# Kernel optimization log

Measured on AMD Instinct MI355X. Metric: run time of the kernel, lower is better.

Reference implementation:

```python
import jax, jax.numpy as jnp
import numpy as np

N_NODES = 50000
N_EDGES = 800000
N_GRAPHS = 64
D = 90


def _kaiming_uniform(key, shape, fan_in):
    # kaiming_uniform_ with nonlinearity='relu': gain=sqrt(2), bound=gain*sqrt(3/fan_in)
    bound = np.sqrt(2.0) * np.sqrt(3.0 / fan_in)
    return jax.random.uniform(key, shape, jnp.float32, -bound, bound)


def setup_inputs() -> dict:
    key = jax.random.key(0)
    ks = jax.random.split(key, 16)
    x = jax.random.normal(ks[0], (N_NODES, D), jnp.float32)
    edge_index = jax.random.randint(ks[1], (2, N_EDGES), 0, N_NODES, jnp.int64)
    batch = jnp.sort(jax.random.randint(ks[2], (N_NODES,), 0, N_GRAPHS, jnp.int64))
    inp = {"x": x, "edge_index": edge_index, "batch": batch}
    # SAGEConv params: lin_l (neighbor path, with bias), lin_r (root path, no bias)
    for i, (kl, kr) in enumerate([(ks[3], ks[4]), (ks[5], ks[6]), (ks[7], ks[8])], start=1):
        inp[f"W{i}l"] = _kaiming_uniform(kl, (D, D), D)
        inp[f"b{i}"] = jnp.zeros((D,), jnp.float32)
        inp[f"W{i}r"] = _kaiming_uniform(kr, (D, D), D)
    inp["Wf1"] = _kaiming_uniform(ks[9], (32, D), D)
    inp["bf1"] = jnp.zeros((32,), jnp.float32)
    inp["Wf2"] = _kaiming_uniform(ks[10], (1, 32), 32)
    inp["bf2"] = jnp.zeros((1,), jnp.float32)
    return inp


def _sage_conv(x, src, dst, Wl, bl, Wr):
    # mean-aggregate neighbor messages x[src] at dst, then lin_l(agg) + lin_r(x)
    msg = x[src]                                           # [E, D] gather
    agg = jax.ops.segment_sum(msg, dst, num_segments=N_NODES)  # [N, D] scatter-add
    deg = jax.ops.segment_sum(jnp.ones((src.shape[0],), x.dtype), dst,
                              num_segments=N_NODES)
    agg = agg / jnp.maximum(deg, 1.0)[:, None]
    return agg @ Wl.T + bl + x @ Wr.T


def reference(x, edge_index, batch, W1l, b1, W1r, W2l, b2, W2r, W3l, b3, W3r,
              Wf1, bf1, Wf2, bf2):
    src, dst = edge_index[0], edge_index[1]
    h = jax.nn.relu(_sage_conv(x, src, dst, W1l, b1, W1r))
    h = jax.nn.relu(_sage_conv(h, src, dst, W2l, b2, W2r))
    h = jax.nn.relu(_sage_conv(h, src, dst, W3l, b3, W3r))
    # global_mean_pool over graph ids
    sums = jax.ops.segment_sum(h, batch, num_segments=N_GRAPHS)      # [G, D]
    cnts = jax.ops.segment_sum(jnp.ones((h.shape[0],), h.dtype), batch,
                               num_segments=N_GRAPHS)
    pooled = sums / jnp.maximum(cnts, 1.0)[:, None]
    h4 = jax.nn.relu(pooled @ Wf1.T + bf1)
    return h4 @ Wf2.T + bf2  # [G, 1]
```

## Files before the change

### kernel.cpp

```cpp
#include <hip/hip_runtime.h>
#include <hip/hip_bf16.h>

#define N_NODES 50000
#define N_PAD   50048
#define N_EDGES 800000
#define N_GRAPHS 64
#define D 90
#define HS  96
#define HSD 48
#define SC  192

#define NBUCKETS 196
#define BSHIFT 8
#define BIN_EPB 4096

typedef __attribute__((ext_vector_type(8))) short bf16x8;
typedef __attribute__((ext_vector_type(4))) float f32x4;

__device__ __forceinline__ float bflo(unsigned int v) { return __uint_as_float(v << 16); }
__device__ __forceinline__ float bfhi(unsigned int v) { return __uint_as_float(v & 0xffff0000u); }
__device__ __forceinline__ unsigned short bf16bits(float f) {
    __hip_bfloat16 b = __float2bfloat16(f);
    return *(unsigned short*)&b;
}
__device__ __forceinline__ unsigned int pack2bf(float lo, float hi) {
    return (unsigned int)bf16bits(lo) | ((unsigned int)bf16bits(hi) << 16);
}

__global__ void k_prep(const float* __restrict__ x, __hip_bfloat16* __restrict__ h0,
                       const float* __restrict__ w1l, const float* __restrict__ w1r,
                       const float* __restrict__ w2l, const float* __restrict__ w2r,
                       const float* __restrict__ w3l, const float* __restrict__ w3r,
                       __hip_bfloat16* __restrict__ Wcat,
                       int* __restrict__ bcnt, float* __restrict__ pooled) {
    int idx = blockIdx.x * 256 + threadIdx.x;
    if (idx < N_PAD * HS) {
        int n = idx / HS, k = idx - n * HS;
        float v = (n < N_NODES && k < D) ? x[n * D + k] : 0.f;
        h0[idx] = __float2bfloat16(v);
    }
    if (idx < 3 * 96 * SC) {
        const int per = 96 * SC;
        int layer = idx / per, rem = idx - layer * per;
        int j = rem / SC, k = rem - j * SC;
        const float* wl = (layer == 0) ? w1l : (layer == 1) ? w2l : w3l;
        const float* wr = (layer == 0) ? w1r : (layer == 1) ? w2r : w3r;
        float v = 0.f;
        if (j < D) {
            if (k < 96) { if (k < D) v = wl[j * D + k]; }
            else        { int kk = k - 96; if (kk < D) v = wr[j * D + kk]; }
        }
        Wcat[idx] = __float2bfloat16(v);
    }
    if (idx < N_GRAPHS * D + N_GRAPHS) pooled[idx] = 0.f;
    if (idx < NBUCKETS) bcnt[idx] = 0;
}

__global__ void k_hist(const int* __restrict__ dst, int* __restrict__ bcnt) {
    __shared__ int h[NBUCKETS];
    int t = threadIdx.x;
    for (int i = t; i < NBUCKETS; i += 256) h[i] = 0;
    __syncthreads();
    int base = blockIdx.x * BIN_EPB;
    int lim = base + BIN_EPB; if (lim > N_EDGES) lim = N_EDGES;
    for (int e = base + t; e < lim; e += 256)
        atomicAdd(&h[dst[e] >> BSHIFT], 1);
    __syncthreads();
    for (int i = t; i < NBUCKETS; i += 256) {
        int c = h[i];
        if (c) atomicAdd(&bcnt[i], c);
    }
}

__global__ void k_bscan(const int* __restrict__ bcnt, int* __restrict__ bbase,
                        int* __restrict__ bcursor) {
    __shared__ int s[256];
    int t = threadIdx.x;
    int v = (t < NBUCKETS) ? bcnt[t] : 0;
    s[t] = v; __syncthreads();
    for (int o = 1; o < 256; o <<= 1) {
        int x = (t >= o) ? s[t - o] : 0;
        __syncthreads();
        s[t] += x;
        __syncthreads();
    }
    int excl = s[t] - v;
    if (t < NBUCKETS) { bbase[t] = excl; bcursor[t] = excl; }
    if (t == 255) bbase[NBUCKETS] = s[255];
}

__global__ __launch_bounds__(256) void k_bin(const int* __restrict__ src,
                                             const int* __restrict__ dst,
                                             int* __restrict__ bcursor,
                                             unsigned int* __restrict__ ebuf) {
    __shared__ int h[NBUCKETS];
    __shared__ int gb[NBUCKETS];
    int t = threadIdx.x;
    for (int i = t; i < NBUCKETS; i += 256) h[i] = 0;
    __syncthreads();
    int base = blockIdx.x * BIN_EPB;
    int sv[16], dv[16], rv[16];
    #pragma unroll
    for (int i = 0; i < 16; ++i) {
        int e = base + i * 256 + t;
        if (e < N_EDGES) {
            sv[i] = src[e];
            dv[i] = dst[e];
            rv[i] = atomicAdd(&h[dv[i] >> BSHIFT], 1);
        }
    }
    __syncthreads();
    for (int i = t; i < NBUCKETS; i += 256)
        gb[i] = h[i] ? atomicAdd(&bcursor[i], h[i]) : 0;
    __syncthreads();
    #pragma unroll
    for (int i = 0; i < 16; ++i) {
        int e = base + i * 256 + t;
        if (e < N_EDGES) {
            int b = dv[i] >> BSHIFT;
            ebuf[gb[b] + rv[i]] = (unsigned int)sv[i] | ((unsigned int)(dv[i] & 255) << 16);
        }
    }
}

__global__ __launch_bounds__(256) void k_fill2(const unsigned int* __restrict__ ebuf,
                                               const int* __restrict__ bbase,
                                               int* __restrict__ off,
                                               int* __restrict__ csr) {
    __shared__ int lcnt[256];
    __shared__ int excl[256];
    int t = threadIdx.x;
    int n0 = blockIdx.x << BSHIFT;
    int ebeg = bbase[blockIdx.x], eend = bbase[blockIdx.x + 1];
    lcnt[t] = 0;
    __syncthreads();
    for (int e = ebeg + t; e < eend; e += 256)
        atomicAdd(&lcnt[ebuf[e] >> 16], 1);
    __syncthreads();
    int v = lcnt[t];
    excl[t] = v; __syncthreads();
    for (int o = 1; o < 256; o <<= 1) {
        int x = (t >= o) ? excl[t - o] : 0;
        __syncthreads();
        excl[t] += x;
        __syncthreads();
    }
    excl[t] -= v;
    int n = n0 + t;
    if (n <= N_NODES) off[n] = ebeg + excl[t];
    lcnt[t] = 0;
    __syncthreads();
    for (int e = ebeg + t; e < eend; e += 256) {
        unsigned int u = ebuf[e];
        int li = u >> 16;
        int r = atomicAdd(&lcnt[li], 1);
        csr[ebeg + excl[li] + r] = (int)(u & 0xFFFFu);
    }
}

__global__ __launch_bounds__(512) void k_layer(
    const unsigned int* __restrict__ hin,
    const __hip_bfloat16* __restrict__ Wcat,
    const float* __restrict__ bias,
    const int* __restrict__ off, const int* __restrict__ csr,
    __hip_bfloat16* __restrict__ hout)
{
    __shared__ unsigned int aggT[64][52];
    __shared__ float biasPad[96];
    int tid = threadIdx.x;
    if (tid < 96) biasPad[tid] = (tid < D) ? bias[tid] : 0.f;
    int w = tid >> 6, lane = tid & 63;

    int eg = lane >> 3, sl = lane & 7;
    int colw = 6 * sl;
    for (int i = 0; i < 8; ++i) {
        int local = w * 8 + i;
        int node = blockIdx.x * 64 + local;
        int beg = 0, end = 0;
        if (node < N_NODES) { beg = off[node]; end = off[node + 1]; }
        float a[12];
        #pragma unroll
        for (int q = 0; q < 12; ++q) a[q] = 0.f;
        int e = beg + eg;
        for (; e + 8 < end; e += 16) {
            int sA = csr[e], sB = csr[e + 8];
            const unsigned int* pA = &hin[sA * HSD + colw];
            const unsigned int* pB = &hin[sB * HSD + colw];
            unsigned int u[6], v[6];
            #pragma unroll
            for (int q = 0; q < 6; ++q) u[q] = pA[q];
            #pragma unroll
            for (int q = 0; q < 6; ++q) v[q] = pB[q];
            #pragma unroll
            for (int q = 0; q < 6; ++q) {
                a[2 * q]     += bflo(u[q]) + bflo(v[q]);
                a[2 * q + 1] += bfhi(u[q]) + bfhi(v[q]);
            }
        }
        if (e < end) {
            const unsigned int* pA = &hin[csr[e] * HSD + colw];
            unsigned int u[6];
            #pragma unroll
            for (int q = 0; q < 6; ++q) u[q] = pA[q];
            #pragma unroll
            for (int q = 0; q < 6; ++q) {
                a[2 * q]     += bflo(u[q]);
                a[2 * q + 1] += bfhi(u[q]);
            }
        }
        #pragma unroll
        for (int m = 8; m <= 32; m <<= 1) {
            #pragma unroll
            for (int q = 0; q < 12; ++q) a[q] += __shfl_xor(a[q], m);
        }
        if (eg == 0) {
            float inv = 1.0f / fmaxf((float)(end - beg), 1.0f);
            #pragma unroll
            for (int q = 0; q < 6; ++q) {
                int c0 = 12 * sl + 2 * q;
                float lo = (c0     < D) ? a[2 * q]     * inv : 0.f;
                float hi = (c0 + 1 < D) ? a[2 * q + 1] * inv : 0.f;
                aggT[local][colw + q] = pack2bf(lo, hi);
            }
        }
    }
    __syncthreads();

    int w4 = w & 3, half = w >> 2;
    int mrow = lane & 15, kg = lane >> 4;
    int r0 = blockIdx.x * 64 + w4 * 16;
    int lrow = w4 * 16 + mrow;
    const short* Wp = (const short*)Wcat;
    const short* Hs = (const short*)hin;

    f32x4 acc[3];
    #pragma unroll
    for (int t = 0; t < 3; ++t) {
        int j = (half * 3 + t) * 16 + mrow;
        float b = biasPad[j];
        acc[t] = (f32x4){b, b, b, b};
    }

    #pragma unroll
    for (int ks = 0; ks < 6; ++ks) {
        bf16x8 afr;
        if (ks < 3) afr = *(const bf16x8*)&aggT[lrow][ks * 16 + kg * 4];
        else        afr = *(const bf16x8*)&Hs[(r0 + mrow) * HS + (ks - 3) * 32 + kg * 8];
        #pragma unroll
        for (int t = 0; t < 3; ++t) {
            int j = (half * 3 + t) * 16 + mrow;
            bf16x8 bfr = *(const bf16x8*)&Wp[j * SC + ks * 32 + kg * 8];
            acc[t] = __builtin_amdgcn_mfma_f32_16x16x32_bf16(afr, bfr, acc[t], 0, 0, 0);
        }
    }

    int orow = r0 + kg * 4;
    #pragma unroll
    for (int t = 0; t < 3; ++t) {
        int j = (half * 3 + t) * 16 + mrow;
        #pragma unroll
        for (int v = 0; v < 4; ++v) {
            float val = (j < D) ? fmaxf(acc[t][v], 0.f) : 0.f;
            hout[(orow + v) * HS + j] = __float2bfloat16(val);
        }
    }
}

#define POOL_WAVES 4096
__global__ void k_pool(const unsigned int* __restrict__ h, const int* __restrict__ batch,
                       float* __restrict__ pooled, float* __restrict__ cntg) {
    int wid  = (blockIdx.x * blockDim.x + threadIdx.x) >> 6;
    int lane = threadIdx.x & 63;
    const int per = (N_NODES + POOL_WAVES - 1) / POOL_WAVES;
    int beg = wid * per;
    int end = beg + per; if (end > N_NODES) end = N_NODES;
    if (beg >= end) return;
    int cur = batch[beg];
    float a0 = 0.f, a1 = 0.f, c = 0.f;
    for (int n = beg; n < end; ++n) {
        int g = batch[n];
        if (g != cur) {
            if (lane < 45) {
                atomicAdd(&pooled[cur * D + 2 * lane], a0);
                atomicAdd(&pooled[cur * D + 2 * lane + 1], a1);
            }
            if (lane == 0) atomicAdd(&cntg[cur], c);
            a0 = a1 = c = 0.f;
            cur = g;
        }
        if (lane < 45) {
            unsigned int v = h[n * HSD + lane];
            a0 += bflo(v);
            a1 += bfhi(v);
        }
        c += 1.f;
    }
    if (lane < 45) {
        atomicAdd(&pooled[cur * D + 2 * lane], a0);
        atomicAdd(&pooled[cur * D + 2 * lane + 1], a1);
    }
    if (lane == 0) atomicAdd(&cntg[cur], c);
}

__global__ void k_mlp(const float* __restrict__ pooled, const float* __restrict__ cntg,
                      const float* __restrict__ Wf1, const float* __restrict__ bf1,
                      const float* __restrict__ Wf2, const float* __restrict__ bf2,
                      float* __restrict__ outp) {
    __shared__ float P[N_GRAPHS][92];
    __shared__ float H4[N_GRAPHS][32];
    int tid = threadIdx.x;
    for (int idx = tid; idx < N_GRAPHS * D; idx += 256) {
        int g = idx / D, d = idx - g * D;
        P[g][d] = pooled[idx] / fmaxf(cntg[g], 1.0f);
    }
    __syncthreads();
    for (int idx = tid; idx < N_GRAPHS * 32; idx += 256) {
        int g = idx >> 5, c = idx & 31;
        float acc = bf1[c];
        for (int d = 0; d < D; ++d) acc += P[g][d] * Wf1[c * D + d];
        H4[g][c] = fmaxf(acc, 0.f);
    }
    __syncthreads();
    if (tid < N_GRAPHS) {
        float acc = bf2[0];
        #pragma unroll
        for (int c = 0; c < 32; ++c) acc += H4[tid][c] * Wf2[c];
        outp[tid] = acc;
    }
}

extern "C" void kernel_launch(void* const* d_in, const int* in_sizes, int n_in,
                              void* d_out, int out_size, void* d_ws, size_t ws_size,
                              hipStream_t stream) {
    const float* x    = (const float*)d_in[0];
    const int*   ei   = (const int*)d_in[1];
    const int*   batch= (const int*)d_in[2];
    const float* W1l  = (const float*)d_in[3];
    const float* b1   = (const float*)d_in[4];
    const float* W1r  = (const float*)d_in[5];
    const float* W2l  = (const float*)d_in[6];
    const float* b2   = (const float*)d_in[7];
    const float* W2r  = (const float*)d_in[8];
    const float* W3l  = (const float*)d_in[9];
    const float* b3   = (const float*)d_in[10];
    const float* W3r  = (const float*)d_in[11];
    const float* Wf1  = (const float*)d_in[12];
    const float* bf1  = (const float*)d_in[13];
    const float* Wf2  = (const float*)d_in[14];
    const float* bf2  = (const float*)d_in[15];
    const int* srcI = ei;
    const int* dstI = ei + N_EDGES;

    char* base = (char*)d_ws;
    size_t o = 0;
    auto alloc = [&](size_t bytes) -> void* {
        void* p = base + o;
        o = (o + bytes + 255) & ~(size_t)255;
        return p;
    };
    int*   bcnt    = (int*)alloc((size_t)NBUCKETS * 4);
    int*   bbase   = (int*)alloc((size_t)(NBUCKETS + 1) * 4);
    int*   bcursor = (int*)alloc((size_t)NBUCKETS * 4);
    int*   off     = (int*)alloc((size_t)(N_NODES + 1) * 4);
    unsigned int* ebuf = (unsigned int*)alloc((size_t)N_EDGES * 4);
    int*   csr     = (int*)alloc((size_t)N_EDGES * 4);
    __hip_bfloat16* hA = (__hip_bfloat16*)alloc((size_t)N_PAD * HS * 2);
    __hip_bfloat16* hB = (__hip_bfloat16*)alloc((size_t)N_PAD * HS * 2);
    __hip_bfloat16* Wcat = (__hip_bfloat16*)alloc((size_t)3 * 96 * SC * 2);
    float* pooled = (float*)alloc((size_t)(N_GRAPHS * D + N_GRAPHS) * 4);
    float* cntg   = pooled + N_GRAPHS * D;

    k_prep<<<(N_PAD * HS + 255) / 256, 256, 0, stream>>>(
        x, hA, W1l, W1r, W2l, W2r, W3l, W3r, Wcat, bcnt, pooled);

    const int EB = (N_EDGES + BIN_EPB - 1) / BIN_EPB;
    k_hist<<<EB, 256, 0, stream>>>(dstI, bcnt);
    k_bscan<<<1, 256, 0, stream>>>(bcnt, bbase, bcursor);
    k_bin<<<EB, 256, 0, stream>>>(srcI, dstI, bcursor, ebuf);
    k_fill2<<<NBUCKETS, 256, 0, stream>>>(ebuf, bbase, off, csr);

    const int LAYER_BLOCKS = N_PAD / 64;

    unsigned int* hAu = (unsigned int*)hA;
    unsigned int* hBu = (unsigned int*)hB;

    k_layer<<<LAYER_BLOCKS, 512, 0, stream>>>(hAu, Wcat,            b1, off, csr, hB);
    k_layer<<<LAYER_BLOCKS, 512, 0, stream>>>(hBu, Wcat +  96 * SC, b2, off, csr, hA);
    k_layer<<<LAYER_BLOCKS, 512, 0, stream>>>(hAu, Wcat + 192 * SC, b3, off, csr, hB);

    k_pool<<<POOL_WAVES / 4, 256, 0, stream>>>(hBu, batch, pooled, cntg);
    k_mlp<<<1, 256, 0, stream>>>(pooled, cntg, Wf1, bf1, Wf2, bf2, (float*)d_out);
}
```

Measured before the change: 240.3 us.

## Store an fp8 copy of node features for the neighbor gather

Each layer now writes an fp8 shadow copy of its output features next to the bf16 copy, and the neighbor-aggregation gather reads the fp8 copy. This halves the bytes moved by the random-access gather, which is the dominant memory cost of the layer kernel. The root-path GEMM still reads bf16. The extra fp8 store adds write traffic and byte-granular stores, and fp8 loses a lot of precision, which may hurt accuracy.

```diff
diff --git a/kernel.cpp b/kernel.cpp
--- a/kernel.cpp
+++ b/kernel.cpp
@@ -8,6 +8,7 @@
 #define D 90
 #define HS  96
 #define HSD 48
+#define HS8 24
 #define SC  192
 
 #define NBUCKETS 196
@@ -16,6 +17,7 @@
 
 typedef __attribute__((ext_vector_type(8))) short bf16x8;
 typedef __attribute__((ext_vector_type(4))) float f32x4;
+typedef __attribute__((ext_vector_type(2))) float f32x2;
 
 __device__ __forceinline__ float bflo(unsigned int v) { return __uint_as_float(v << 16); }
 __device__ __forceinline__ float bfhi(unsigned int v) { return __uint_as_float(v & 0xffff0000u); }
@@ -26,8 +28,13 @@
 __device__ __forceinline__ unsigned int pack2bf(float lo, float hi) {
     return (unsigned int)bf16bits(lo) | ((unsigned int)bf16bits(hi) << 16);
 }
+__device__ __forceinline__ unsigned char f32_to_fp8(float v) {
+    int pk = __builtin_amdgcn_cvt_pk_fp8_f32(v, v, 0, false);
+    return (unsigned char)(pk & 0xff);
+}
 
 __global__ void k_prep(const float* __restrict__ x, __hip_bfloat16* __restrict__ h0,
+                       unsigned char* __restrict__ h8,
                        const float* __restrict__ w1l, const float* __restrict__ w1r,
                        const float* __restrict__ w2l, const float* __restrict__ w2r,
                        const float* __restrict__ w3l, const float* __restrict__ w3r,
@@ -38,6 +45,7 @@
         int n = idx / HS, k = idx - n * HS;
         float v = (n < N_NODES && k < D) ? x[n * D + k] : 0.f;
         h0[idx] = __float2bfloat16(v);
+        h8[idx] = f32_to_fp8(v);
     }
     if (idx < 3 * 96 * SC) {
         const int per = 96 * SC;
@@ -160,10 +168,12 @@
 
 __global__ __launch_bounds__(512) void k_layer(
     const unsigned int* __restrict__ hin,
+    const unsigned int* __restrict__ hin8,
     const __hip_bfloat16* __restrict__ Wcat,
     const float* __restrict__ bias,
     const int* __restrict__ off, const int* __restrict__ csr,
-    __hip_bfloat16* __restrict__ hout)
+    __hip_bfloat16* __restrict__ hout,
+    unsigned char* __restrict__ hout8)
 {
     __shared__ unsigned int aggT[64][52];
     __shared__ float biasPad[96];
@@ -172,7 +182,7 @@
     int w = tid >> 6, lane = tid & 63;
 
     int eg = lane >> 3, sl = lane & 7;
-    int colw = 6 * sl;
+    int col8 = 3 * sl;
     for (int i = 0; i < 8; ++i) {
         int local = w * 8 + i;
         int node = blockIdx.x * 64 + local;
@@ -181,33 +191,46 @@
         float a[12];
         #pragma unroll
         for (int q = 0; q < 12; ++q) a[q] = 0.f;
+
         int e = beg + eg;
         for (; e + 8 < end; e += 16) {
             int sA = csr[e], sB = csr[e + 8];
-            const unsigned int* pA = &hin[sA * HSD + colw];
-            const unsigned int* pB = &hin[sB * HSD + colw];
-            unsigned int u[6], v[6];
-            #pragma unroll
-            for (int q = 0; q < 6; ++q) u[q] = pA[q];
-            #pragma unroll
-            for (int q = 0; q < 6; ++q) v[q] = pB[q];
-            #pragma unroll
-            for (int q = 0; q < 6; ++q) {
-                a[2 * q]     += bflo(u[q]) + bflo(v[q]);
-                a[2 * q + 1] += bfhi(u[q]) + bfhi(v[q]);
+            const unsigned int* pA = &hin8[sA * HS8 + col8];
+            const unsigned int* pB = &hin8[sB * HS8 + col8];
+            unsigned int u[3], v[3];
+            #pragma unroll
+            for (int q = 0; q < 3; ++q) u[q] = pA[q];
+            #pragma unroll
+            for (int q = 0; q < 3; ++q) v[q] = pB[q];
+            #pragma unroll
+            for (int q = 0; q < 3; ++q) {
+                f32x2 lo = __builtin_amdgcn_cvt_pk_f32_fp8((int)u[q], false);
+                f32x2 hi = __builtin_amdgcn_cvt_pk_f32_fp8((int)u[q], true);
+                a[4 * q]     += lo.x; a[4 * q + 1] += lo.y;
+                a[4 * q + 2] += hi.x; a[4 * q + 3] += hi.y;
             }
+            #pragma unroll
+            for (int q = 0; q < 3; ++q) {
+                f32x2 lo = __builtin_amdgcn_cvt_pk_f32_fp8((int)v[q], false);
+                f32x2 hi = __builtin_amdgcn_cvt_pk_f32_fp8((int)v[q], true);
+                a[4 * q]     += lo.x; a[4 * q + 1] += lo.y;
+                a[4 * q + 2] += hi.x; a[4 * q + 3] += hi.y;
+            }
         }
         if (e < end) {
-            const unsigned int* pA = &hin[csr[e] * HSD + colw];
-            unsigned int u[6];
-            #pragma unroll
-            for (int q = 0; q < 6; ++q) u[q] = pA[q];
-            #pragma unroll
-            for (int q = 0; q < 6; ++q) {
-                a[2 * q]     += bflo(u[q]);
-                a[2 * q + 1] += bfhi(u[q]);
+            const unsigned int* pA = &hin8[csr[e] * HS8 + col8];
+            unsigned int u[3];
+            #pragma unroll
+            for (int q = 0; q < 3; ++q) u[q] = pA[q];
+            #pragma unroll
+            for (int q = 0; q < 3; ++q) {
+                f32x2 lo = __builtin_amdgcn_cvt_pk_f32_fp8((int)u[q], false);
+                f32x2 hi = __builtin_amdgcn_cvt_pk_f32_fp8((int)u[q], true);
+                a[4 * q]     += lo.x; a[4 * q + 1] += lo.y;
+                a[4 * q + 2] += hi.x; a[4 * q + 3] += hi.y;
             }
         }
+
         #pragma unroll
         for (int m = 8; m <= 32; m <<= 1) {
             #pragma unroll
@@ -220,7 +243,7 @@
                 int c0 = 12 * sl + 2 * q;
                 float lo = (c0     < D) ? a[2 * q]     * inv : 0.f;
                 float hi = (c0 + 1 < D) ? a[2 * q + 1] * inv : 0.f;
-                aggT[local][colw + q] = pack2bf(lo, hi);
+                aggT[local][6 * sl + q] = pack2bf(lo, hi);
             }
         }
     }
@@ -262,6 +285,7 @@
         for (int v = 0; v < 4; ++v) {
             float val = (j < D) ? fmaxf(acc[t][v], 0.f) : 0.f;
             hout[(orow + v) * HS + j] = __float2bfloat16(val);
+            hout8[(orow + v) * HS + j] = f32_to_fp8(val);
         }
     }
 }
@@ -366,12 +390,14 @@
     int*   csr     = (int*)alloc((size_t)N_EDGES * 4);
     __hip_bfloat16* hA = (__hip_bfloat16*)alloc((size_t)N_PAD * HS * 2);
     __hip_bfloat16* hB = (__hip_bfloat16*)alloc((size_t)N_PAD * HS * 2);
+    unsigned char* h8A = (unsigned char*)alloc((size_t)N_PAD * HS);
+    unsigned char* h8B = (unsigned char*)alloc((size_t)N_PAD * HS);
     __hip_bfloat16* Wcat = (__hip_bfloat16*)alloc((size_t)3 * 96 * SC * 2);
     float* pooled = (float*)alloc((size_t)(N_GRAPHS * D + N_GRAPHS) * 4);
     float* cntg   = pooled + N_GRAPHS * D;
 
     k_prep<<<(N_PAD * HS + 255) / 256, 256, 0, stream>>>(
-        x, hA, W1l, W1r, W2l, W2r, W3l, W3r, Wcat, bcnt, pooled);
+        x, hA, h8A, W1l, W1r, W2l, W2r, W3l, W3r, Wcat, bcnt, pooled);
 
     const int EB = (N_EDGES + BIN_EPB - 1) / BIN_EPB;
     k_hist<<<EB, 256, 0, stream>>>(dstI, bcnt);
@@ -381,12 +407,14 @@
 
     const int LAYER_BLOCKS = N_PAD / 64;
 
-    unsigned int* hAu = (unsigned int*)hA;
-    unsigned int* hBu = (unsigned int*)hB;
-
-    k_layer<<<LAYER_BLOCKS, 512, 0, stream>>>(hAu, Wcat,            b1, off, csr, hB);
-    k_layer<<<LAYER_BLOCKS, 512, 0, stream>>>(hBu, Wcat +  96 * SC, b2, off, csr, hA);
-    k_layer<<<LAYER_BLOCKS, 512, 0, stream>>>(hAu, Wcat + 192 * SC, b3, off, csr, hB);
+    unsigned int* hAu  = (unsigned int*)hA;
+    unsigned int* hBu  = (unsigned int*)hB;
+    unsigned int* h8Au = (unsigned int*)h8A;
+    unsigned int* h8Bu = (unsigned int*)h8B;
+
+    k_layer<<<LAYER_BLOCKS, 512, 0, stream>>>(hAu, h8Au, Wcat,            b1, off, csr, hB, h8B);
+    k_layer<<<LAYER_BLOCKS, 512, 0, stream>>>(hBu, h8Bu, Wcat +  96 * SC, b2, off, csr, hA, h8A);
+    k_layer<<<LAYER_BLOCKS, 512, 0, stream>>>(hAu, h8Au, Wcat + 192 * SC, b3, off, csr, hB, h8B);
 
     k_pool<<<POOL_WAVES / 4, 256, 0, stream>>>(hBu, batch, pooled, cntg);
     k_mlp<<<1, 256, 0, stream>>>(pooled, cntg, Wf1, bf1, Wf2, bf2, (float*)d_out);
```

Measured after the change: 248.3 us. +3.3%, slower.

## Assign one node per 8-lane group in layer aggregation, shrink blocks

Applied to the files above, without the earlier changes.

Layer aggregation now gives each node its own 8-lane group, which walks all of that node's edges serially with a 4-way unrolled gather. Previously the whole wave processed one node at a time, spreading edges across 8 groups and then reducing with cross-lane shuffles. The shuffle reduction and the serial per-node loop are removed, and blocks shrink to 32 nodes and 256 threads so the MFMA stage maps 2 row-tiles per block. The trade-off is that uneven degrees now cause load imbalance between groups in a wave, and each group holds more loads in flight.

```diff
diff --git a/kernel.cpp b/kernel.cpp
--- a/kernel.cpp
+++ b/kernel.cpp
@@ -158,78 +158,81 @@
     }
 }
 
-__global__ __launch_bounds__(512) void k_layer(
+__global__ __launch_bounds__(256) void k_layer(
     const unsigned int* __restrict__ hin,
     const __hip_bfloat16* __restrict__ Wcat,
     const float* __restrict__ bias,
     const int* __restrict__ off, const int* __restrict__ csr,
     __hip_bfloat16* __restrict__ hout)
 {
-    __shared__ unsigned int aggT[64][52];
+    __shared__ unsigned int aggT[32][52];
     __shared__ float biasPad[96];
     int tid = threadIdx.x;
     if (tid < 96) biasPad[tid] = (tid < D) ? bias[tid] : 0.f;
     int w = tid >> 6, lane = tid & 63;
 
-    int eg = lane >> 3, sl = lane & 7;
+    int grp = lane >> 3, sl = lane & 7;
+    int local = w * 8 + grp;
+    int node = blockIdx.x * 32 + local;
     int colw = 6 * sl;
-    for (int i = 0; i < 8; ++i) {
-        int local = w * 8 + i;
-        int node = blockIdx.x * 64 + local;
-        int beg = 0, end = 0;
-        if (node < N_NODES) { beg = off[node]; end = off[node + 1]; }
-        float a[12];
-        #pragma unroll
-        for (int q = 0; q < 12; ++q) a[q] = 0.f;
-        int e = beg + eg;
-        for (; e + 8 < end; e += 16) {
-            int sA = csr[e], sB = csr[e + 8];
-            const unsigned int* pA = &hin[sA * HSD + colw];
-            const unsigned int* pB = &hin[sB * HSD + colw];
-            unsigned int u[6], v[6];
-            #pragma unroll
-            for (int q = 0; q < 6; ++q) u[q] = pA[q];
-            #pragma unroll
-            for (int q = 0; q < 6; ++q) v[q] = pB[q];
-            #pragma unroll
-            for (int q = 0; q < 6; ++q) {
-                a[2 * q]     += bflo(u[q]) + bflo(v[q]);
-                a[2 * q + 1] += bfhi(u[q]) + bfhi(v[q]);
-            }
-        }
-        if (e < end) {
-            const unsigned int* pA = &hin[csr[e] * HSD + colw];
-            unsigned int u[6];
-            #pragma unroll
-            for (int q = 0; q < 6; ++q) u[q] = pA[q];
-            #pragma unroll
-            for (int q = 0; q < 6; ++q) {
-                a[2 * q]     += bflo(u[q]);
-                a[2 * q + 1] += bfhi(u[q]);
-            }
-        }
-        #pragma unroll
-        for (int m = 8; m <= 32; m <<= 1) {
-            #pragma unroll
-            for (int q = 0; q < 12; ++q) a[q] += __shfl_xor(a[q], m);
-        }
-        if (eg == 0) {
-            float inv = 1.0f / fmaxf((float)(end - beg), 1.0f);
-            #pragma unroll
-            for (int q = 0; q < 6; ++q) {
-                int c0 = 12 * sl + 2 * q;
-                float lo = (c0     < D) ? a[2 * q]     * inv : 0.f;
-                float hi = (c0 + 1 < D) ? a[2 * q + 1] * inv : 0.f;
-                aggT[local][colw + q] = pack2bf(lo, hi);
-            }
-        }
-    }
-    __syncthreads();
-
-    int w4 = w & 3, half = w >> 2;
+
+    int beg = 0, end = 0;
+    if (node < N_NODES) { beg = off[node]; end = off[node + 1]; }
+
+    float a[12];
+    #pragma unroll
+    for (int q = 0; q < 12; ++q) a[q] = 0.f;
+
+    int e = beg;
+    for (; e + 4 <= end; e += 4) {
+        int s0 = csr[e], s1 = csr[e + 1], s2 = csr[e + 2], s3 = csr[e + 3];
+        const unsigned int* p0 = &hin[s0 * HSD + colw];
+        const unsigned int* p1 = &hin[s1 * HSD + colw];
+        const unsigned int* p2 = &hin[s2 * HSD + colw];
+        const unsigned int* p3 = &hin[s3 * HSD + colw];
+        unsigned int u0[6], u1[6], u2[6], u3[6];
+        #pragma unroll
+        for (int q = 0; q < 6; ++q) u0[q] = p0[q];
+        #pragma unroll
+        for (int q = 0; q < 6; ++q) u1[q] = p1[q];
+        #pragma unroll
+        for (int q = 0; q < 6; ++q) u2[q] = p2[q];
+        #pragma unroll
+        for (int q = 0; q < 6; ++q) u3[q] = p3[q];
+        #pragma unroll
+        for (int q = 0; q < 6; ++q) {
+            a[2 * q]     += (bflo(u0[q]) + bflo(u1[q])) + (bflo(u2[q]) + bflo(u3[q]));
+            a[2 * q + 1] += (bfhi(u0[q]) + bfhi(u1[q])) + (bfhi(u2[q]) + bfhi(u3[q]));
+        }
+    }
+    for (; e < end; ++e) {
+        const unsigned int* p0 = &hin[csr[e] * HSD + colw];
+        unsigned int u0[6];
+        #pragma unroll
+        for (int q = 0; q < 6; ++q) u0[q] = p0[q];
+        #pragma unroll
+        for (int q = 0; q < 6; ++q) {
+            a[2 * q]     += bflo(u0[q]);
+            a[2 * q + 1] += bfhi(u0[q]);
+        }
+    }
+
+    {
+        float inv = 1.0f / fmaxf((float)(end - beg), 1.0f);
+        #pragma unroll
+        for (int q = 0; q < 6; ++q) {
+            int c0 = 12 * sl + 2 * q;
+            float lo = (c0     < D) ? a[2 * q]     * inv : 0.f;
+            float hi = (c0 + 1 < D) ? a[2 * q + 1] * inv : 0.f;
+            aggT[local][colw + q] = pack2bf(lo, hi);
+        }
+    }
+    __syncthreads();
+
+    int w2 = w & 1, half = w >> 1;
     int mrow = lane & 15, kg = lane >> 4;
-    int r0 = blockIdx.x * 64 + w4 * 16;
-    int lrow = w4 * 16 + mrow;
+    int r0 = blockIdx.x * 32 + w2 * 16;
+    int lrow = w2 * 16 + mrow;
     const short* Wp = (const short*)Wcat;
     const short* Hs = (const short*)hin;
 
@@ -379,14 +382,14 @@
     k_bin<<<EB, 256, 0, stream>>>(srcI, dstI, bcursor, ebuf);
     k_fill2<<<NBUCKETS, 256, 0, stream>>>(ebuf, bbase, off, csr);
 
-    const int LAYER_BLOCKS = N_PAD / 64;
+    const int LAYER_BLOCKS = N_PAD / 32;
 
     unsigned int* hAu = (unsigned int*)hA;
     unsigned int* hBu = (unsigned int*)hB;
 
-    k_layer<<<LAYER_BLOCKS, 512, 0, stream>>>(hAu, Wcat,            b1, off, csr, hB);
-    k_layer<<<LAYER_BLOCKS, 512, 0, stream>>>(hBu, Wcat +  96 * SC, b2, off, csr, hA);
-    k_layer<<<LAYER_BLOCKS, 512, 0, stream>>>(hAu, Wcat + 192 * SC, b3, off, csr, hB);
+    k_layer<<<LAYER_BLOCKS, 256, 0, stream>>>(hAu, Wcat,            b1, off, csr, hB);
+    k_layer<<<LAYER_BLOCKS, 256, 0, stream>>>(hBu, Wcat +  96 * SC, b2, off, csr, hA);
+    k_layer<<<LAYER_BLOCKS, 256, 0, stream>>>(hAu, Wcat + 192 * SC, b3, off, csr, hB);
 
     k_pool<<<POOL_WAVES / 4, 256, 0, stream>>>(hBu, batch, pooled, cntg);
     k_mlp<<<1, 256, 0, stream>>>(pooled, cntg, Wf1, bf1, Wf2, bf2, (float*)d_out);
```

New measurement: 217.4 us. -9.5%, faster.
